# Kernel tuning notes

Measured on AMD Instinct MI355X. Metric: run time of the kernel, lower is better.

## Reference

```python
import jax, jax.numpy as jnp
import numpy as np

B, L, D = 2, 4096, 1024
H, DK, DV = 4, 256, 256
CONV_K = 4
FIR_KS = (1, 3, 7, 15)
GQP = 128
NS = len(FIR_KS) + 2  # fir scales + delta path + direct value path
GIN = GQP + NS
GH = max(8, GIN)
CHUNK = 32
FLOOR = 0.02  # step 0 -> floor_start


def l2norm(x):
    return x * jax.lax.rsqrt(jnp.sum(x * x, -1, keepdims=True) + 1e-6)


def dw_causal_conv(x, w):
    # x: (B, L, C), w: (C, K) depthwise causal conv (ShortConvolution / FIR)
    K = w.shape[1]
    y = jax.lax.conv_general_dilated(
        jnp.moveaxis(x, 1, 2), w[:, None, :], (1,), [(K - 1, 0)],
        feature_group_count=w.shape[0],
        dimension_numbers=("NCH", "OIH", "NCH"))
    return jnp.moveaxis(y, 1, 2)


def delta_rule_chunkwise(q, k, v, beta):
    # q,k: (b,h,L,dk)  v: (b,h,L,dv)  beta: (b,h,L);  L % CHUNK == 0
    b, h, Lp, dk = q.shape
    dv = v.shape[-1]
    n = Lp // CHUNK
    q = l2norm(q)
    k = l2norm(k)
    v = v * beta[..., None]
    kb = k * beta[..., None]
    rs = lambda t: t.reshape(b, h, n, CHUNK, -1)
    q, k, v, kb = rs(q), rs(k), rs(v), rs(kb)
    tri = jnp.triu(jnp.ones((CHUNK, CHUNK), bool), 0)       # incl diag
    tri_s = jnp.triu(jnp.ones((CHUNK, CHUNK), bool), 1)     # strict upper
    # inv = -(k_beta k^T) masked to strictly-lower
    inv = -jnp.where(tri, 0.0, jnp.einsum('bhncd,bhned->bhnce', kb, k))
    # forward substitution: (I - A)^{-1} - I for strictly lower A
    for i in range(1, CHUNK):
        row = inv[:, :, :, i, :]                              # (b,h,n,C)
        upd = jnp.einsum('bhnk,bhnkj->bhnj', row, inv)        # zero for j>=i
        inv = inv.at[:, :, :, i, :].add(upd)
    inv = inv + jnp.eye(CHUNK, dtype=inv.dtype)
    inv = inv.astype(jnp.bfloat16).astype(q.dtype)
    u = inv @ v                                               # (b,h,n,C,dv)
    w = inv @ kb                                              # (b,h,n,C,dk)
    mv = lambda t: jnp.moveaxis(t, 2, 0)                      # -> (n,b,h,C,d)
    S0 = jnp.zeros((b, h, dk, dv), q.dtype)

    def step(S, xs):
        q_i, k_i, u_i, w_i = xs
        attn = jnp.where(tri_s, 0.0, q_i @ jnp.swapaxes(k_i, -1, -2))
        u_t = u_i - w_i @ S
        o = q_i @ S + attn @ u_t
        S = S + jnp.swapaxes(k_i, -1, -2) @ u_t
        return S, o

    _, out = jax.lax.scan(step, S0, (mv(q), mv(k), mv(u), mv(w)))
    return jnp.moveaxis(out, 0, 2).reshape(b, h, Lp, dv)


def rmsnorm(x, w, eps=1e-5):
    return x * jax.lax.rsqrt(jnp.mean(x * x, -1, keepdims=True) + eps) * w


def _dirac_fir(key, channels, k):
    w = jnp.zeros((channels, k), jnp.float32).at[:, -1].set(1.0)
    return w + 0.01 * jax.random.normal(key, (channels, k), jnp.float32)


def setup_inputs():
    key = jax.random.key(0)
    ks = jax.random.split(key, 24)
    sc = 0.02
    C = H * DV
    b2 = jnp.zeros((NS,), jnp.float32).at[-1].set(1.0)  # identity-path bias
    return {
        "hidden_states": jax.random.normal(ks[0], (B, L, D), jnp.float32),
        "Wq": jax.random.normal(ks[1], (D, H * DK), jnp.float32) * sc,
        "Wk": jax.random.normal(ks[2], (D, H * DK), jnp.float32) * sc,
        "Wv": jax.random.normal(ks[3], (D, H * DV), jnp.float32) * sc,
        "Wb": jax.random.normal(ks[4], (D, H), jnp.float32) * sc,
        "conv_q_w": jax.random.normal(ks[5], (H * DK, CONV_K), jnp.float32) * 0.1,
        "conv_k_w": jax.random.normal(ks[6], (H * DK, CONV_K), jnp.float32) * 0.1,
        "conv_v_w": jax.random.normal(ks[7], (H * DV, CONV_K), jnp.float32) * 0.1,
        "fir_w0": _dirac_fir(ks[8], C, FIR_KS[0]),
        "fir_w1": _dirac_fir(ks[9], C, FIR_KS[1]),
        "fir_w2": _dirac_fir(ks[10], C, FIR_KS[2]),
        "fir_w3": _dirac_fir(ks[11], C, FIR_KS[3]),
        "Wqg": jax.random.normal(ks[12], (D, GQP), jnp.float32) * sc,
        "bqg": jnp.zeros((GQP,), jnp.float32),
        "Wf1": jax.random.normal(ks[13], (GIN, GH), jnp.float32) * sc,
        "bf1": jnp.zeros((GH,), jnp.float32),
        "Wf2": jax.random.normal(ks[14], (GH, NS), jnp.float32) * sc,
        "bf2": b2,
        "log_temp": jnp.zeros((H,), jnp.float32),
        "o_norm_w": jnp.ones((DV,), jnp.float32),
        "Wo": jax.random.normal(ks[15], (H * DV, D), jnp.float32) * sc,
    }


def reference(hidden_states, Wq, Wk, Wv, Wb, conv_q_w, conv_k_w, conv_v_w,
              fir_w0, fir_w1, fir_w2, fir_w3, Wqg, bqg, Wf1, bf1, Wf2, bf2,
              log_temp, o_norm_w, Wo):
    x = hidden_states
    # projections + causal ShortConvolution with SiLU (qk_activation='silu')
    q = jax.nn.silu(dw_causal_conv(x @ Wq, conv_q_w))
    k = jax.nn.silu(dw_causal_conv(x @ Wk, conv_k_w))
    v = jax.nn.silu(dw_causal_conv(x @ Wv, conv_v_w))
    q = q.reshape(B, L, H, DK)
    k = k.reshape(B, L, H, DK)
    v_direct = v.reshape(B, L, H, DV)
    beta = jax.nn.sigmoid(x @ Wb)  # (B,L,H)
    bh = lambda t: jnp.swapaxes(t, 1, 2)  # (B,L,H,d) -> (B,H,L,d)
    delta_bh = delta_rule_chunkwise(bh(q), bh(k), bh(v_direct), jnp.swapaxes(beta, 1, 2))
    delta_out = jnp.swapaxes(delta_bh, 1, 2)  # (B,L,H,DV)
    # multi-scale depthwise causal FIR branches on the value stream
    v_flat = v_direct.reshape(B, L, H * DV)
    firs = [dw_causal_conv(v_flat, w).reshape(B, L, H, DV)
            for w in (fir_w0, fir_w1, fir_w2, fir_w3)]
    streams = jnp.stack(firs + [delta_out, v_direct], axis=3)  # (B,L,H,NS,DV)
    # query-conditioned summary router
    summaries = jnp.mean(streams, axis=-1)                     # (B,L,H,NS)
    qg = x @ Wqg + bqg                                         # (B,L,GQP)
    qg = jnp.broadcast_to(qg[:, :, None, :], (B, L, H, GQP))
    gate_in = jnp.concatenate([qg, summaries], axis=-1)        # (B,L,H,GIN)
    hmid = jax.nn.gelu(gate_in @ Wf1 + bf1, approximate=False)
    logits = (hmid @ Wf2 + bf2) / jnp.exp(log_temp)[None, None, :, None]
    p = jax.nn.softmax(logits, axis=-1)
    p = p * (1.0 - NS * FLOOR) + FLOOR                          # prob floor
    fused = jnp.einsum('blhs,blhsd->blhd', p, streams)
    o = rmsnorm(fused, o_norm_w)
    return o.reshape(B, L, H * DV) @ Wo
```

## Files before the change

### kernel.cpp

```cpp
#include <hip/hip_runtime.h>
#include <hip/hip_bf16.h>
#include <math.h>

#define B_ 2
#define L_ 4096
#define D_ 1024
#define H_ 4
#define DK_ 256
#define BL_ 8192
#define C_ 1024
#define NCH_ 128
#define GQP_c 128
#define NS_c 6
#define GIN_c 134
#define GH_c 134

typedef __attribute__((ext_vector_type(8))) short short8;
typedef __attribute__((ext_vector_type(4))) float f32x4;

__device__ __forceinline__ float block_sum256(float v, float* red) {
  int t = threadIdx.x;
  #pragma unroll
  for (int o = 32; o > 0; o >>= 1) v += __shfl_down(v, o, 64);
  __syncthreads();
  if ((t & 63) == 0) red[t >> 6] = v;
  __syncthreads();
  return red[0] + red[1] + red[2] + red[3];
}

__device__ __forceinline__ unsigned short bf16bits(float f) {
  __hip_bfloat16 h = __float2bfloat16(f);
  return *(unsigned short*)&h;
}

__device__ __forceinline__ float bits2f(unsigned short u) {
  unsigned int x = ((unsigned int)u) << 16;
  return *(float*)&x;
}

__device__ __forceinline__ float4 fma4(float4 a, float4 b, float4 c) {
  return make_float4(fmaf(a.x, b.x, c.x), fmaf(a.y, b.y, c.y),
                     fmaf(a.z, b.z, c.z), fmaf(a.w, b.w, c.w));
}

__device__ __forceinline__ void gload_lds16(const void* g, void* l) {
  __builtin_amdgcn_global_load_lds(
      (const __attribute__((address_space(1))) void*)g,
      (__attribute__((address_space(3))) void*)l, 16, 0, 0);
}

__global__ __launch_bounds__(256) void f32_to_bf16_k(const float* __restrict__ in,
    __hip_bfloat16* __restrict__ out) {
  size_t i = ((size_t)blockIdx.x * 256 + threadIdx.x) << 2;
  float4 v = *(const float4*)(in + i);
  ushort4 o;
  o.x = bf16bits(v.x); o.y = bf16bits(v.y); o.z = bf16bits(v.z); o.w = bf16bits(v.w);
  *(ushort4*)((unsigned short*)out + i) = o;
}

__global__ __launch_bounds__(256) void transpose_bf16(const float* __restrict__ W,
    __hip_bfloat16* __restrict__ WT, int K, int N) {
  __shared__ float tile[32][33];
  int t = threadIdx.x;
  int r = t >> 3, c4 = (t & 7) << 2;
  int n0 = blockIdx.x << 5, k0 = blockIdx.y << 5;
  float4 v = *(const float4*)(W + (size_t)(k0 + r) * N + n0 + c4);
  tile[r][c4] = v.x; tile[r][c4 + 1] = v.y; tile[r][c4 + 2] = v.z; tile[r][c4 + 3] = v.w;
  __syncthreads();
  ushort4 o;
  o.x = bf16bits(tile[c4][r]);
  o.y = bf16bits(tile[c4 + 1][r]);
  o.z = bf16bits(tile[c4 + 2][r]);
  o.w = bf16bits(tile[c4 + 3][r]);
  *(ushort4*)((unsigned short*)WT + (size_t)(n0 + r) * K + k0 + c4) = o;
}

__global__ __launch_bounds__(256) void small_transpose(const float* __restrict__ in,
    float* __restrict__ out, int R, int Cc, int OS) {
  int total = Cc * OS;
  for (int e = blockIdx.x * 256 + threadIdx.x; e < total; e += gridDim.x * 256) {
    int cIdx = e / OS, r = e - cIdx * OS;
    out[e] = (r < R) ? in[(size_t)r * Cc + cIdx] : 0.f;
  }
}

__global__ __launch_bounds__(256) void wf1q_prep(const float* __restrict__ Wf1,
    __hip_bfloat16* __restrict__ out) {
  int idx = blockIdx.x * 256 + threadIdx.x;
  int u = idx >> 7, i = idx & 127;
  float val = (u < GH_c) ? Wf1[i * GH_c + u] : 0.f;
  out[idx] = __float2bfloat16(val);
}

__global__ __launch_bounds__(256) void conv_prep(const float* __restrict__ cw,
    float* __restrict__ cwT) {
  int t = blockIdx.x * 256 + threadIdx.x;
  int j = t >> 10, c = t & (C_ - 1);
  cwT[t] = cw[(c << 2) + j];
}

__global__ __launch_bounds__(256) void gemm_bf16(
    const __hip_bfloat16* __restrict__ A, const __hip_bfloat16* __restrict__ BT,
    const float* __restrict__ bias, float* __restrict__ C, int M, int N, int K) {
  __shared__ __align__(16) __hip_bfloat16 Asm[4096];
  __shared__ __align__(16) __hip_bfloat16 Bsm[4096];
  int tid = threadIdx.x;
  int lane = tid & 63, wave = tid >> 6;
  int wm = wave >> 1, wn = wave & 1;
  int rowBase = blockIdx.y * 128, colBase = blockIdx.x * 128;
  f32x4 acc[4][4];
  #pragma unroll
  for (int i = 0; i < 4; ++i)
    #pragma unroll
    for (int j = 0; j < 4; ++j) acc[i][j] = (f32x4){0.f, 0.f, 0.f, 0.f};

  for (int kt = 0; kt < K; kt += 32) {
    __syncthreads();
    #pragma unroll
    for (int it = 0; it < 2; ++it) {
      int s = tid + (it << 8);
      int T = s >> 6, q = (s >> 4) & 3, m = s & 15;
      const __hip_bfloat16* ga = A + (size_t)(rowBase + T * 16 + m) * K + kt + q * 8;
      gload_lds16(ga, Asm + s * 8);
      const __hip_bfloat16* gb = BT + (size_t)(colBase + T * 16 + m) * K + kt + q * 8;
      gload_lds16(gb, Bsm + s * 8);
    }
    __syncthreads();
    short8 af[4], bfr[4];
    #pragma unroll
    for (int i = 0; i < 4; ++i) {
      af[i]  = *(const short8*)(Asm + ((wm * 4 + i) << 9) + lane * 8);
      bfr[i] = *(const short8*)(Bsm + ((wn * 4 + i) << 9) + lane * 8);
    }
    #pragma unroll
    for (int i = 0; i < 4; ++i)
      #pragma unroll
      for (int j = 0; j < 4; ++j)
        acc[i][j] = __builtin_amdgcn_mfma_f32_16x16x32_bf16(af[i], bfr[j], acc[i][j], 0, 0, 0);
  }
  int r0 = (lane >> 4) * 4, c0 = lane & 15;
  #pragma unroll
  for (int i = 0; i < 4; ++i) {
    int row = rowBase + (wm * 4 + i) * 16 + r0;
    #pragma unroll
    for (int j = 0; j < 4; ++j) {
      int col = colBase + (wn * 4 + j) * 16 + c0;
      float bs = bias ? bias[col] : 0.f;
      #pragma unroll
      for (int r = 0; r < 4; ++r)
        C[(size_t)(row + r) * N + col] = acc[i][j][r] + bs;
    }
  }
}

__global__ __launch_bounds__(256) void conv_silu_v4(const float* __restrict__ in,
    const float* __restrict__ wT, float* __restrict__ out) {
  int f = blockIdx.x * 256 + threadIdx.x;
  int e = f << 2;
  int c = e & (C_ - 1);
  int l = (e >> 10) & (L_ - 1);
  float4 acc = make_float4(0.f, 0.f, 0.f, 0.f);
  #pragma unroll
  for (int j = 0; j < 4; ++j) {
    int ll = l - 3 + j;
    if (ll >= 0) {
      float4 vj = *(const float4*)(in + e + ((j - 3) << 10));
      float4 wj = *(const float4*)(wT + (j << 10) + c);
      acc = fma4(wj, vj, acc);
    }
  }
  float4 o;
  o.x = acc.x / (1.f + expf(-acc.x));
  o.y = acc.y / (1.f + expf(-acc.y));
  o.z = acc.z / (1.f + expf(-acc.z));
  o.w = acc.w / (1.f + expf(-acc.w));
  *(float4*)(out + e) = o;
}

__global__ __launch_bounds__(256) void beta_kernel(const float* __restrict__ x,
    const float* __restrict__ Wb, float* __restrict__ beta) {
  int row = blockIdx.x;
  int t = threadIdx.x;
  int h = t >> 6, lane = t & 63;
  const float* xr = x + (size_t)row * D_;
  float acc = 0.f;
  for (int k = lane; k < D_; k += 64) acc += xr[k] * Wb[(k << 2) + h];
  #pragma unroll
  for (int o = 32; o > 0; o >>= 1) acc += __shfl_down(acc, o, 64);
  if (lane == 0) beta[(row << 2) + h] = 1.f / (1.f + expf(-acc));
}

__global__ __launch_bounds__(256) void precompute(const float* __restrict__ q,
    const float* __restrict__ k, const float* __restrict__ v,
    const float* __restrict__ beta,
    float* __restrict__ qn, float* __restrict__ kn,
    float* __restrict__ vb, float* __restrict__ kb) {
  __shared__ float red[4];
  int bid = blockIdx.x;
  int t = threadIdx.x;
  int b = bid >> 14;
  int h = (bid >> 12) & 3;
  int l = bid & (L_ - 1);
  size_t in_off = (((size_t)(b * L_ + l)) << 10) + (h << 8) + t;
  float qv = q[in_off], kv = k[in_off], vv = v[in_off];
  float sq = block_sum256(qv * qv, red);
  float sk = block_sum256(kv * kv, red);
  float rq = rsqrtf(sq + 1e-6f);
  float rk = rsqrtf(sk + 1e-6f);
  float bt = beta[((b * L_ + l) << 2) + h];
  size_t oo = ((size_t)bid << 8) + t;
  float knv = kv * rk;
  qn[oo] = qv * rq;
  kn[oo] = knv;
  vb[oo] = vv * bt;
  kb[oo] = knv * bt;
}

__global__ __launch_bounds__(256) void inv_attn(const float* __restrict__ qn,
    const float* kn, const float* __restrict__ kb,
    float* __restrict__ invb, __hip_bfloat16* __restrict__ att_bf,
    __hip_bfloat16* knT_bf) {
  __shared__ float kn_s[32][257];
  __shared__ float inv_s[32][33];
  int ci = blockIdx.x;
  int t = threadIdx.x;
  size_t base = ((size_t)ci) << 13;
  for (int e = t; e < 8192; e += 256) kn_s[e >> 8][e & 255] = kn[base + e];
  __syncthreads();
  {
    unsigned short tmp[32];
    #pragma unroll
    for (int j = 0; j < 32; ++j) tmp[j] = bf16bits(kn_s[j][t]);
    unsigned short* kd = (unsigned short*)knT_bf + (((size_t)ci) << 14) +
                         (size_t)(t >> 4) * 512 + (size_t)(t & 15) * 8;
    #pragma unroll
    for (int g = 0; g < 4; ++g) *(uint4*)(kd + g * 128) = ((const uint4*)tmp)[g];
  }
  {
    int r = t >> 3, kt = t & 7;
    const float4* qrow = (const float4*)(qn + base + (size_t)r * 256 + (kt << 5));
    unsigned short tmp[32];
    #pragma unroll
    for (int i = 0; i < 8; ++i) {
      float4 f = qrow[i];
      tmp[i * 4 + 0] = bf16bits(f.x); tmp[i * 4 + 1] = bf16bits(f.y);
      tmp[i * 4 + 2] = bf16bits(f.z); tmp[i * 4 + 3] = bf16bits(f.w);
    }
    unsigned short* qd = (unsigned short*)knT_bf + (((size_t)ci) << 14) + 8192 +
                         (size_t)(((r >> 4) << 3) + kt) * 512 + (size_t)(r & 15) * 8;
    #pragma unroll
    for (int g = 0; g < 4; ++g) *(uint4*)(qd + g * 128) = ((const uint4*)tmp)[g];
  }
  #pragma unroll
  for (int p = 0; p < 4; ++p) {
    int e = t + (p << 8);
    int i = e >> 5, j = e & 31;
    const float* kbi = kb + base + (i << 8);
    const float* qni = qn + base + (i << 8);
    float am = 0.f, aa = 0.f;
    for (int kk = 0; kk < 256; ++kk) {
      float knv = kn_s[j][kk];
      am += kbi[kk] * knv;
      aa += qni[kk] * knv;
    }
    inv_s[i][j] = (j < i) ? -am : 0.f;
    ((unsigned short*)att_bf)[((size_t)ci << 10) + (size_t)(i >> 4) * 512 +
        (size_t)((i & 15) + ((j >> 3) << 4)) * 8 + (j & 7)] =
        bf16bits((j <= i) ? aa : 0.f);
  }
  __syncthreads();
  for (int i = 1; i < 32; ++i) {
    float upd = 0.f;
    if (t < i) {
      for (int kk = t + 1; kk < i; ++kk) upd += inv_s[i][kk] * inv_s[kk][t];
    }
    __syncthreads();
    if (t < i) inv_s[i][t] += upd;
    __syncthreads();
  }
  #pragma unroll
  for (int p = 0; p < 4; ++p) {
    int e = t + (p << 8);
    int i = e >> 5, j = e & 31;
    float val = inv_s[i][j] + (i == j ? 1.f : 0.f);
    val = __bfloat162float(__float2bfloat16(val));
    invb[((size_t)ci << 10) + e] = val;
  }
}

__global__ __launch_bounds__(256) void uw_kernel(const float* __restrict__ invb,
    float* __restrict__ vb_u, float* kb_w, __hip_bfloat16* w_bf) {
  __shared__ float inv_s[32][33];
  __shared__ float tile[32][260];
  int ci = blockIdx.x, t = threadIdx.x;
  size_t base = ((size_t)ci) << 13;
  for (int e = t; e < 1024; e += 256) inv_s[e >> 5][e & 31] = invb[((size_t)ci << 10) + e];
  for (int ph = 0; ph < 2; ++ph) {
    const float* src = (ph == 0) ? vb_u : kb_w;
    __syncthreads();
    for (int f = t; f < 2048; f += 256) {
      int e = f << 2;
      *(float4*)&tile[e >> 8][e & 255] = *(const float4*)(src + base + e);
    }
    __syncthreads();
    int c4 = (t & 63) << 2;
    int ig = t >> 6;
    float4 acc[8];
    #pragma unroll
    for (int ii = 0; ii < 8; ++ii) acc[ii] = make_float4(0.f, 0.f, 0.f, 0.f);
    for (int j = 0; j < 32; ++j) {
      float4 v4 = *(const float4*)&tile[j][c4];
      #pragma unroll
      for (int ii = 0; ii < 8; ++ii) {
        float iv = inv_s[(ig << 3) + ii][j];
        acc[ii].x += iv * v4.x; acc[ii].y += iv * v4.y;
        acc[ii].z += iv * v4.z; acc[ii].w += iv * v4.w;
      }
    }
    #pragma unroll
    for (int ii = 0; ii < 8; ++ii) {
      int i = (ig << 3) + ii;
      if (ph == 0) {
        *(float4*)(vb_u + base + (i << 8) + c4) = acc[ii];
      } else {
        ushort4 o;
        o.x = bf16bits(-acc[ii].x); o.y = bf16bits(-acc[ii].y);
        o.z = bf16bits(-acc[ii].z); o.w = bf16bits(-acc[ii].w);
        unsigned short* wd = (unsigned short*)w_bf + (((size_t)ci) << 14) +
            (size_t)(((i >> 4) << 3) + (c4 >> 5)) * 512 +
            (size_t)((i & 15) + (((c4 >> 3) & 3) << 4)) * 8 + (c4 & 7);
        *(ushort4*)wd = o;
      }
    }
  }
}

__global__ __launch_bounds__(64, 1) void scan_kernel(
    const __hip_bfloat16* __restrict__ w_bf,
    const __hip_bfloat16* __restrict__ kq_bf,
    const __hip_bfloat16* __restrict__ att_bf,
    const float* __restrict__ u, float* __restrict__ dout) {
  __shared__ __align__(16) unsigned short Sim[2][2][16 * 264];
  __shared__ __align__(16) float UtT[16 * 36];
  int lane = threadIdx.x;
  int mlane = lane & 15, quad = lane >> 4;
  int bh = blockIdx.x & 7;
  int cb = blockIdx.x >> 3;
  int cbase = cb << 4;

  const unsigned short* wbase = (const unsigned short*)w_bf;
  const unsigned short* kqbase = (const unsigned short*)kq_bf;
  const unsigned short* abase = (const unsigned short*)att_bf;

  short8 Wr[16], Qr[16], Kr[16], Ar[2];
  float ur[8], urn[8];

  auto load_WQ = [&](int nc) {
    size_t cb14 = ((size_t)(bh * NCH_ + nc)) << 14;
    const short8* wg = (const short8*)(wbase + cb14 + (size_t)lane * 8);
    const short8* qg = (const short8*)(kqbase + cb14 + 8192 + (size_t)lane * 8);
    #pragma unroll
    for (int s = 0; s < 16; ++s) { Wr[s] = wg[s * 64]; Qr[s] = qg[s * 64]; }
  };
  auto load_K = [&](int nc) {
    size_t cb14 = ((size_t)(bh * NCH_ + nc)) << 14;
    const short8* kg = (const short8*)(kqbase + cb14 + (size_t)lane * 8);
    #pragma unroll
    for (int s = 0; s < 16; ++s) Kr[s] = kg[s * 64];
  };
  auto load_A = [&](int nc) {
    const short8* ag = (const short8*)(abase + (((size_t)(bh * NCH_ + nc)) << 10) +
                                       (size_t)lane * 8);
    Ar[0] = ag[0]; Ar[1] = ag[64];
  };
  auto load_u8 = [&](int nc, float* dst) {
    size_t cbf = ((size_t)(bh * NCH_ + nc)) << 13;
    const float* up = u + cbf + (size_t)(quad * 4) * 256 + cbase + mlane;
    #pragma unroll
    for (int tt = 0; tt < 2; ++tt)
      #pragma unroll
      for (int r = 0; r < 4; ++r) dst[tt * 4 + r] = up[(tt * 16 + r) * 256];
  };

  for (int e = lane; e < 16 * 264; e += 64) { Sim[0][0][e] = 0; Sim[0][1][e] = 0; }
  f32x4 accS[16];
  #pragma unroll
  for (int i = 0; i < 16; ++i) accS[i] = (f32x4){0.f, 0.f, 0.f, 0.f};

  load_WQ(0);
  load_K(0);
  load_A(0);
  load_u8(0, ur);

  for (int nc = 0; nc < NCH_; ++nc) {
    int cur = nc & 1, alt = cur ^ 1;
    int nn = nc + 1 < NCH_ ? nc + 1 : NCH_ - 1;

    f32x4 uh0 = (f32x4){ur[0], ur[1], ur[2], ur[3]};
    f32x4 uh1 = (f32x4){ur[4], ur[5], ur[6], ur[7]};
    f32x4 ul0 = (f32x4){0.f, 0.f, 0.f, 0.f}, ul1 = (f32x4){0.f, 0.f, 0.f, 0.f};
    f32x4 oh0 = (f32x4){0.f, 0.f, 0.f, 0.f}, oh1 = (f32x4){0.f, 0.f, 0.f, 0.f};
    f32x4 ol0 = (f32x4){0.f, 0.f, 0.f, 0.f}, ol1 = (f32x4){0.f, 0.f, 0.f, 0.f};
    #pragma unroll
    for (int kt = 0; kt < 8; ++kt) {
      short8 bhi = *(const short8*)&Sim[cur][0][mlane * 264 + kt * 32 + quad * 8];
      short8 blo = *(const short8*)&Sim[cur][1][mlane * 264 + kt * 32 + quad * 8];
      uh0 = __builtin_amdgcn_mfma_f32_16x16x32_bf16(Wr[kt], bhi, uh0, 0, 0, 0);
      ul0 = __builtin_amdgcn_mfma_f32_16x16x32_bf16(Wr[kt], blo, ul0, 0, 0, 0);
      uh1 = __builtin_amdgcn_mfma_f32_16x16x32_bf16(Wr[8 + kt], bhi, uh1, 0, 0, 0);
      ul1 = __builtin_amdgcn_mfma_f32_16x16x32_bf16(Wr[8 + kt], blo, ul1, 0, 0, 0);
      oh0 = __builtin_amdgcn_mfma_f32_16x16x32_bf16(Qr[kt], bhi, oh0, 0, 0, 0);
      ol0 = __builtin_amdgcn_mfma_f32_16x16x32_bf16(Qr[kt], blo, ol0, 0, 0, 0);
      oh1 = __builtin_amdgcn_mfma_f32_16x16x32_bf16(Qr[8 + kt], bhi, oh1, 0, 0, 0);
      ol1 = __builtin_amdgcn_mfma_f32_16x16x32_bf16(Qr[8 + kt], blo, ol1, 0, 0, 0);
    }
    f32x4 ut0 = uh0 + ul0, ut1 = uh1 + ul1;
    *(f32x4*)&UtT[mlane * 36 + quad * 4] = ut0;
    *(f32x4*)&UtT[mlane * 36 + 16 + quad * 4] = ut1;
    load_WQ(nn);
    load_u8(nn, urn);
    short8 but;
    {
      const float* up = &UtT[mlane * 36 + quad * 8];
      #pragma unroll
      for (int j = 0; j < 8; ++j) but[j] = (short)bf16bits(up[j]);
    }
    f32x4 o0 = oh0 + ol0, o1 = oh1 + ol1;
    o0 = __builtin_amdgcn_mfma_f32_16x16x32_bf16(Ar[0], but, o0, 0, 0, 0);
    o1 = __builtin_amdgcn_mfma_f32_16x16x32_bf16(Ar[1], but, o1, 0, 0, 0);
    load_A(nn);
    size_t cbf = ((size_t)(bh * NCH_ + nc)) << 13;
    float* op = dout + cbf + (size_t)(quad * 4) * 256 + cbase + mlane;
    #pragma unroll
    for (int r = 0; r < 4; ++r) { op[r * 256] = o0[r]; op[(16 + r) * 256] = o1[r]; }
    #pragma unroll
    for (int t2 = 0; t2 < 16; ++t2) {
      accS[t2] = __builtin_amdgcn_mfma_f32_16x16x32_bf16(Kr[t2], but, accS[t2], 0, 0, 0);
      unsigned short nh[4], nl[4];
      #pragma unroll
      for (int r = 0; r < 4; ++r) {
        float sv = accS[t2][r];
        unsigned short hb = bf16bits(sv);
        nh[r] = hb;
        nl[r] = bf16bits(sv - bits2f(hb));
      }
      *(uint2*)&Sim[alt][0][mlane * 264 + t2 * 16 + quad * 4] = *(const uint2*)nh;
      *(uint2*)&Sim[alt][1][mlane * 264 + t2 * 16 + quad * 4] = *(const uint2*)nl;
    }
    load_K(nn);
    #pragma unroll
    for (int r = 0; r < 8; ++r) ur[r] = urn[r];
  }
}

__global__ __launch_bounds__(256, 1) void gate_kernel(
    const float* __restrict__ v, const float* __restrict__ delta,
    const float* __restrict__ qgH,
    const float* __restrict__ fw0, const float* __restrict__ fw1T,
    const float* __restrict__ fw2T, const float* __restrict__ fw3T,
    const float* __restrict__ Wf1, const float* __restrict__ Wf2,
    const float* __restrict__ bf1, const float* __restrict__ bf2,
    const float* __restrict__ ltm, const float* __restrict__ onw,
    __hip_bfloat16* __restrict__ obf) {
  __shared__ float W1t[6][136];
  __shared__ float W2f[804];
  __shared__ float bf1s[136];
  int t = threadIdx.x;
  int wave = t >> 6, lane = t & 63;
  for (int e = t; e < 804; e += 256) {
    int s = e / 134, u = e - s * 134;
    W1t[s][u] = Wf1[(128 + s) * GH_c + u];
    W2f[e] = Wf2[e];
  }
  if (t < GH_c) bf1s[t] = bf1[t];
  __syncthreads();

  int bid = blockIdx.x;
  int bl0 = (((bid & 7) << 7) | (bid >> 3)) << 3;
  int b = bl0 >> 12;
  int h = wave;
  int c = (h << 8) + (lane << 2);

  float4 fw3r[15], fw2r[7], fw1r[3], fw0r;
  #pragma unroll
  for (int j = 0; j < 15; ++j) fw3r[j] = *(const float4*)(fw3T + (j << 10) + c);
  #pragma unroll
  for (int j = 0; j < 7; ++j) fw2r[j] = *(const float4*)(fw2T + (j << 10) + c);
  #pragma unroll
  for (int j = 0; j < 3; ++j) fw1r[j] = *(const float4*)(fw1T + (j << 10) + c);
  fw0r = *(const float4*)(fw0 + c);
  float4 ow = *(const float4*)(onw + (lane << 2));
  float itemp = expf(ltm[h]);
  float b2r[6];
  #pragma unroll
  for (int s = 0; s < 6; ++s) b2r[s] = bf2[s];
  int u3 = 128 + (lane < 6 ? lane : 0);

  auto gelu = [](float a) -> float {
    return 0.5f * a * (1.f + erff(a * 0.70710678f));
  };

  for (int tk = 0; tk < 8; ++tk) {
    int bl = bl0 + tk;
    int l = bl & (L_ - 1);
    float4 st0, st1, st2, st3, st4, st5;
    st1 = make_float4(0, 0, 0, 0);
    st2 = make_float4(0, 0, 0, 0);
    st3 = make_float4(0, 0, 0, 0);
    #pragma unroll
    for (int j = 0; j < 15; ++j) {
      int ll = l - 14 + j;
      float4 vj = make_float4(0, 0, 0, 0);
      if (ll >= 0) vj = *(const float4*)(v + ((((size_t)(b * L_ + ll)) << 10) + c));
      st3 = fma4(fw3r[j], vj, st3);
      if (j >= 8) st2 = fma4(fw2r[j - 8], vj, st2);
      if (j >= 12) st1 = fma4(fw1r[j - 12], vj, st1);
      if (j == 14) {
        st0 = make_float4(fw0r.x * vj.x, fw0r.y * vj.y, fw0r.z * vj.z, fw0r.w * vj.w);
        st5 = vj;
      }
    }
    st4 = *(const float4*)(delta + ((((size_t)((b * H_ + h) * L_ + l)) << 8) + (lane << 2)));

    float s0 = st0.x + st0.y + st0.z + st0.w;
    float s1 = st1.x + st1.y + st1.z + st1.w;
    float s2 = st2.x + st2.y + st2.z + st2.w;
    float s3 = st3.x + st3.y + st3.z + st3.w;
    float s4 = st4.x + st4.y + st4.z + st4.w;
    float s5 = st5.x + st5.y + st5.z + st5.w;
    #pragma unroll
    for (int o = 32; o > 0; o >>= 1) {
      s0 += __shfl_down(s0, o, 64); s1 += __shfl_down(s1, o, 64);
      s2 += __shfl_down(s2, o, 64); s3 += __shfl_down(s3, o, 64);
      s4 += __shfl_down(s4, o, 64); s5 += __shfl_down(s5, o, 64);
    }
    float ss_[6];
    ss_[0] = __shfl(s0, 0, 64) * (1.f / 256.f);
    ss_[1] = __shfl(s1, 0, 64) * (1.f / 256.f);
    ss_[2] = __shfl(s2, 0, 64) * (1.f / 256.f);
    ss_[3] = __shfl(s3, 0, 64) * (1.f / 256.f);
    ss_[4] = __shfl(s4, 0, 64) * (1.f / 256.f);
    ss_[5] = __shfl(s5, 0, 64) * (1.f / 256.f);

    const float* qr = qgH + ((size_t)bl << 8);
    float a0 = qr[lane] + bf1s[lane];
    float a1 = qr[64 + lane] + bf1s[64 + lane];
    float a2 = qr[u3] + bf1s[u3];
    #pragma unroll
    for (int s = 0; s < 6; ++s) {
      a0 = fmaf(W1t[s][lane], ss_[s], a0);
      a1 = fmaf(W1t[s][64 + lane], ss_[s], a1);
      a2 = fmaf(W1t[s][u3], ss_[s], a2);
    }
    float h0 = gelu(a0);
    float h1 = gelu(a1);
    float h2 = (lane < 6) ? gelu(a2) : 0.f;

    const float* w2a = W2f + lane * 6;
    const float* w2b = W2f + (64 + lane) * 6;
    const float* w2c = W2f + u3 * 6;
    float t0 = h0 * w2a[0] + h1 * w2b[0] + h2 * w2c[0];
    float t1 = h0 * w2a[1] + h1 * w2b[1] + h2 * w2c[1];
    float t2 = h0 * w2a[2] + h1 * w2b[2] + h2 * w2c[2];
    float t3 = h0 * w2a[3] + h1 * w2b[3] + h2 * w2c[3];
    float t4 = h0 * w2a[4] + h1 * w2b[4] + h2 * w2c[4];
    float t5 = h0 * w2a[5] + h1 * w2b[5] + h2 * w2c[5];
    #pragma unroll
    for (int o = 32; o > 0; o >>= 1) {
      t0 += __shfl_down(t0, o, 64); t1 += __shfl_down(t1, o, 64);
      t2 += __shfl_down(t2, o, 64); t3 += __shfl_down(t3, o, 64);
      t4 += __shfl_down(t4, o, 64); t5 += __shfl_down(t5, o, 64);
    }
    float p0, p1, p2, p3, p4, p5;
    if (lane == 0) {
      float l0v = (t0 + b2r[0]) / itemp, l1v = (t1 + b2r[1]) / itemp;
      float l2v = (t2 + b2r[2]) / itemp, l3v = (t3 + b2r[3]) / itemp;
      float l4v = (t4 + b2r[4]) / itemp, l5v = (t5 + b2r[5]) / itemp;
      float m = fmaxf(fmaxf(fmaxf(l0v, l1v), fmaxf(l2v, l3v)), fmaxf(l4v, l5v));
      float e0 = expf(l0v - m), e1 = expf(l1v - m), e2 = expf(l2v - m);
      float e3 = expf(l3v - m), e4 = expf(l4v - m), e5 = expf(l5v - m);
      float inv = 1.f / (e0 + e1 + e2 + e3 + e4 + e5);
      p0 = e0 * inv * 0.88f + 0.02f; p1 = e1 * inv * 0.88f + 0.02f;
      p2 = e2 * inv * 0.88f + 0.02f; p3 = e3 * inv * 0.88f + 0.02f;
      p4 = e4 * inv * 0.88f + 0.02f; p5 = e5 * inv * 0.88f + 0.02f;
    }
    p0 = __shfl(p0, 0, 64); p1 = __shfl(p1, 0, 64); p2 = __shfl(p2, 0, 64);
    p3 = __shfl(p3, 0, 64); p4 = __shfl(p4, 0, 64); p5 = __shfl(p5, 0, 64);

    float4 fu;
    fu.x = p0 * st0.x + p1 * st1.x + p2 * st2.x + p3 * st3.x + p4 * st4.x + p5 * st5.x;
    fu.y = p0 * st0.y + p1 * st1.y + p2 * st2.y + p3 * st3.y + p4 * st4.y + p5 * st5.y;
    fu.z = p0 * st0.z + p1 * st1.z + p2 * st2.z + p3 * st3.z + p4 * st4.z + p5 * st5.z;
    fu.w = p0 * st0.w + p1 * st1.w + p2 * st2.w + p3 * st3.w + p4 * st4.w + p5 * st5.w;
    float ssq = fu.x * fu.x + fu.y * fu.y + fu.z * fu.z + fu.w * fu.w;
    #pragma unroll
    for (int o = 32; o > 0; o >>= 1) ssq += __shfl_xor(ssq, o, 64);
    float sc = rsqrtf(ssq * (1.f / 256.f) + 1e-5f);
    ushort4 ob;
    ob.x = bf16bits(fu.x * sc * ow.x);
    ob.y = bf16bits(fu.y * sc * ow.y);
    ob.z = bf16bits(fu.z * sc * ow.z);
    ob.w = bf16bits(fu.w * sc * ow.w);
    *(ushort4*)((unsigned short*)obf + (((size_t)bl) << 10) + c) = ob;
  }
}

extern "C" void kernel_launch(void* const* d_in, const int* in_sizes, int n_in,
                              void* d_out, int out_size, void* d_ws, size_t ws_size,
                              hipStream_t stream) {
  const float* x   = (const float*)d_in[0];
  const float* Wq  = (const float*)d_in[1];
  const float* Wk  = (const float*)d_in[2];
  const float* Wv  = (const float*)d_in[3];
  const float* Wb  = (const float*)d_in[4];
  const float* cqw = (const float*)d_in[5];
  const float* ckw = (const float*)d_in[6];
  const float* cvw = (const float*)d_in[7];
  const float* fw0 = (const float*)d_in[8];
  const float* fw1 = (const float*)d_in[9];
  const float* fw2 = (const float*)d_in[10];
  const float* fw3 = (const float*)d_in[11];
  const float* Wqg = (const float*)d_in[12];
  const float* bqg = (const float*)d_in[13];
  const float* Wf1 = (const float*)d_in[14];
  const float* bf1 = (const float*)d_in[15];
  const float* Wf2 = (const float*)d_in[16];
  const float* bf2 = (const float*)d_in[17];
  const float* ltm = (const float*)d_in[18];
  const float* onw = (const float*)d_in[19];
  const float* Wo  = (const float*)d_in[20];
  float* out = (float*)d_out;
  float* ws = (float*)d_ws;

  const size_t BIG = (size_t)BL_ * C_;
  float* qpre = ws;
  float* kpre = ws + BIG;
  float* vpre = ws + 2 * BIG;
  float* qs   = ws + 3 * BIG;
  float* ks   = ws + 4 * BIG;
  float* vs   = ws + 5 * BIG;
  float* kbw  = ws + 6 * BIG;
  float* invb = ws + 7 * BIG;
  float* attb = invb + (size_t)1024 * 1024;
  float* beta = attb + (size_t)1024 * 1024;
  float* qg   = beta + (size_t)BL_ * H_;

  __hip_bfloat16* x_bf  = (__hip_bfloat16*)qs;
  __hip_bfloat16* wqT   = (__hip_bfloat16*)kbw;
  __hip_bfloat16* wkT   = wqT + (size_t)1024 * 1024;
  __hip_bfloat16* wvT   = wkT + (size_t)1024 * 1024;
  __hip_bfloat16* wqgT  = wvT + (size_t)1024 * 1024;
  __hip_bfloat16* woT   = (__hip_bfloat16*)kbw;
  __hip_bfloat16* gate_bf = (__hip_bfloat16*)qpre;
  __hip_bfloat16* knT_bf = (__hip_bfloat16*)kpre;
  __hip_bfloat16* w_bf   = (__hip_bfloat16*)kbw;
  __hip_bfloat16* att_bf = (__hip_bfloat16*)attb;
  float* scr   = attb + (size_t)600000;
  float* fw1T  = scr;
  float* fw2T  = scr + 3072;
  float* fw3T  = scr + 10240;
  float* cqwT  = scr + 25600;
  float* ckwT  = scr + 29696;
  float* cvwT  = scr + 33792;

  float* qgH = ks;
  __hip_bfloat16* qg_bf  = (__hip_bfloat16*)(ks + (size_t)3 * 1024 * 1024);
  __hip_bfloat16* wf1qT  = (__hip_bfloat16*)(ks + (size_t)4 * 1024 * 1024);

  dim3 blk(256);
  f32_to_bf16_k<<<dim3(BL_ * D_ / 1024), blk, 0, stream>>>(x, x_bf);
  transpose_bf16<<<dim3(32, 32), blk, 0, stream>>>(Wq, wqT, D_, C_);
  transpose_bf16<<<dim3(32, 32), blk, 0, stream>>>(Wk, wkT, D_, C_);
  transpose_bf16<<<dim3(32, 32), blk, 0, stream>>>(Wv, wvT, D_, C_);
  transpose_bf16<<<dim3(4, 32), blk, 0, stream>>>(Wqg, wqgT, D_, GQP_c);
  small_transpose<<<dim3(16), blk, 0, stream>>>(fw1, fw1T, 1024, 3, 1024);
  small_transpose<<<dim3(32), blk, 0, stream>>>(fw2, fw2T, 1024, 7, 1024);
  small_transpose<<<dim3(64), blk, 0, stream>>>(fw3, fw3T, 1024, 15, 1024);
  conv_prep<<<dim3(16), blk, 0, stream>>>(cqw, cqwT);
  conv_prep<<<dim3(16), blk, 0, stream>>>(ckw, ckwT);
  conv_prep<<<dim3(16), blk, 0, stream>>>(cvw, cvwT);
  gemm_bf16<<<dim3(8, 64), blk, 0, stream>>>(x_bf, wqT, nullptr, qpre, BL_, C_, D_);
  gemm_bf16<<<dim3(8, 64), blk, 0, stream>>>(x_bf, wkT, nullptr, kpre, BL_, C_, D_);
  gemm_bf16<<<dim3(8, 64), blk, 0, stream>>>(x_bf, wvT, nullptr, vpre, BL_, C_, D_);
  gemm_bf16<<<dim3(1, 64), blk, 0, stream>>>(x_bf, wqgT, bqg, qg, BL_, GQP_c, D_);
  beta_kernel<<<dim3(BL_), blk, 0, stream>>>(x, Wb, beta);
  conv_silu_v4<<<dim3(BL_ * C_ / 1024), blk, 0, stream>>>(qpre, cqwT, qs);
  conv_silu_v4<<<dim3(BL_ * C_ / 1024), blk, 0, stream>>>(kpre, ckwT, ks);
  conv_silu_v4<<<dim3(BL_ * C_ / 1024), blk, 0, stream>>>(vpre, cvwT, vs);
  precompute<<<dim3(B_ * H_ * L_), blk, 0, stream>>>(qs, ks, vs, beta, qpre, kpre,
                                                     vpre, kbw);
  f32_to_bf16_k<<<dim3(BL_ * GQP_c / 1024), blk, 0, stream>>>(qg, qg_bf);
  wf1q_prep<<<dim3(128), blk, 0, stream>>>(Wf1, wf1qT);
  gemm_bf16<<<dim3(2, 64), blk, 0, stream>>>(qg_bf, wf1qT, nullptr, qgH, BL_, 256, 128);
  inv_attn<<<dim3(1024), blk, 0, stream>>>(qpre, kpre, kbw, invb, att_bf, knT_bf);
  uw_kernel<<<dim3(1024), blk, 0, stream>>>(invb, vpre, kbw, w_bf);
  scan_kernel<<<dim3(128), dim3(64), 0, stream>>>(w_bf, knT_bf, att_bf, vpre, qs);
  transpose_bf16<<<dim3(32, 32), blk, 0, stream>>>(Wo, woT, C_, D_);
  gate_kernel<<<dim3(1024), blk, 0, stream>>>(vs, qs, qgH, fw0, fw1T, fw2T, fw3T,
                                              Wf1, Wf2, bf1, bf2, ltm, onw, gate_bf);
  gemm_bf16<<<dim3(8, 64), blk, 0, stream>>>(gate_bf, woT, nullptr, out, BL_, D_, C_);
}
```

Measured before the change: 943.8 us.

## Fuse causal conv, SiLU and L2 norm; apply beta on the fly downstream

```diff
diff --git a/kernel.cpp b/kernel.cpp
--- a/kernel.cpp
+++ b/kernel.cpp
@@ -18,16 +18,6 @@
 typedef __attribute__((ext_vector_type(8))) short short8;
 typedef __attribute__((ext_vector_type(4))) float f32x4;
 
-__device__ __forceinline__ float block_sum256(float v, float* red) {
-  int t = threadIdx.x;
-  #pragma unroll
-  for (int o = 32; o > 0; o >>= 1) v += __shfl_down(v, o, 64);
-  __syncthreads();
-  if ((t & 63) == 0) red[t >> 6] = v;
-  __syncthreads();
-  return red[0] + red[1] + red[2] + red[3];
-}
-
 __device__ __forceinline__ unsigned short bf16bits(float f) {
   __hip_bfloat16 h = __float2bfloat16(f);
   return *(unsigned short*)&h;
@@ -41,6 +31,11 @@
 __device__ __forceinline__ float4 fma4(float4 a, float4 b, float4 c) {
   return make_float4(fmaf(a.x, b.x, c.x), fmaf(a.y, b.y, c.y),
                      fmaf(a.z, b.z, c.z), fmaf(a.w, b.w, c.w));
+}
+
+__device__ __forceinline__ float4 silu4(float4 a) {
+  return make_float4(a.x / (1.f + expf(-a.x)), a.y / (1.f + expf(-a.y)),
+                     a.z / (1.f + expf(-a.z)), a.w / (1.f + expf(-a.w)));
 }
 
 __device__ __forceinline__ void gload_lds16(const void* g, void* l) {
@@ -153,30 +148,6 @@
   }
 }
 
-__global__ __launch_bounds__(256) void conv_silu_v4(const float* __restrict__ in,
-    const float* __restrict__ wT, float* __restrict__ out) {
-  int f = blockIdx.x * 256 + threadIdx.x;
-  int e = f << 2;
-  int c = e & (C_ - 1);
-  int l = (e >> 10) & (L_ - 1);
-  float4 acc = make_float4(0.f, 0.f, 0.f, 0.f);
-  #pragma unroll
-  for (int j = 0; j < 4; ++j) {
-    int ll = l - 3 + j;
-    if (ll >= 0) {
-      float4 vj = *(const float4*)(in + e + ((j - 3) << 10));
-      float4 wj = *(const float4*)(wT + (j << 10) + c);
-      acc = fma4(wj, vj, acc);
-    }
-  }
-  float4 o;
-  o.x = acc.x / (1.f + expf(-acc.x));
-  o.y = acc.y / (1.f + expf(-acc.y));
-  o.z = acc.z / (1.f + expf(-acc.z));
-  o.w = acc.w / (1.f + expf(-acc.w));
-  *(float4*)(out + e) = o;
-}
-
 __global__ __launch_bounds__(256) void beta_kernel(const float* __restrict__ x,
     const float* __restrict__ Wb, float* __restrict__ beta) {
   int row = blockIdx.x;
@@ -190,41 +161,59 @@
   if (lane == 0) beta[(row << 2) + h] = 1.f / (1.f + expf(-acc));
 }
 
-__global__ __launch_bounds__(256) void precompute(const float* __restrict__ q,
-    const float* __restrict__ k, const float* __restrict__ v,
-    const float* __restrict__ beta,
-    float* __restrict__ qn, float* __restrict__ kn,
-    float* __restrict__ vb, float* __restrict__ kb) {
-  __shared__ float red[4];
+__global__ __launch_bounds__(256) void conv_norm_fused(
+    const float* __restrict__ qpre, const float* __restrict__ kpre,
+    const float* __restrict__ vpre,
+    const float* __restrict__ cqwT, const float* __restrict__ ckwT,
+    const float* __restrict__ cvwT,
+    float* __restrict__ vs, float* __restrict__ qn, float* __restrict__ kn) {
   int bid = blockIdx.x;
+  int b = bid >> 12, l = bid & (L_ - 1);
   int t = threadIdx.x;
-  int b = bid >> 14;
-  int h = (bid >> 12) & 3;
-  int l = bid & (L_ - 1);
-  size_t in_off = (((size_t)(b * L_ + l)) << 10) + (h << 8) + t;
-  float qv = q[in_off], kv = k[in_off], vv = v[in_off];
-  float sq = block_sum256(qv * qv, red);
-  float sk = block_sum256(kv * kv, red);
-  float rq = rsqrtf(sq + 1e-6f);
-  float rk = rsqrtf(sk + 1e-6f);
-  float bt = beta[((b * L_ + l) << 2) + h];
-  size_t oo = ((size_t)bid << 8) + t;
-  float knv = kv * rk;
-  qn[oo] = qv * rq;
-  kn[oo] = knv;
-  vb[oo] = vv * bt;
-  kb[oo] = knv * bt;
+  int h = t >> 6, lane = t & 63;
+  int c = t << 2;
+  float4 qa = make_float4(0.f, 0.f, 0.f, 0.f);
+  float4 ka = make_float4(0.f, 0.f, 0.f, 0.f);
+  float4 va = make_float4(0.f, 0.f, 0.f, 0.f);
+  #pragma unroll
+  for (int j = 0; j < 4; ++j) {
+    int ll = l - 3 + j;
+    if (ll >= 0) {
+      size_t roff = (((size_t)(b * L_ + ll)) << 10) + c;
+      qa = fma4(*(const float4*)(cqwT + (j << 10) + c), *(const float4*)(qpre + roff), qa);
+      ka = fma4(*(const float4*)(ckwT + (j << 10) + c), *(const float4*)(kpre + roff), ka);
+      va = fma4(*(const float4*)(cvwT + (j << 10) + c), *(const float4*)(vpre + roff), va);
+    }
+  }
+  float4 qv = silu4(qa), kv = silu4(ka), vv = silu4(va);
+  *(float4*)(vs + (((size_t)bid) << 10) + c) = vv;
+  float sq = qv.x * qv.x + qv.y * qv.y + qv.z * qv.z + qv.w * qv.w;
+  float sk = kv.x * kv.x + kv.y * kv.y + kv.z * kv.z + kv.w * kv.w;
+  #pragma unroll
+  for (int o = 32; o > 0; o >>= 1) {
+    sq += __shfl_xor(sq, o, 64);
+    sk += __shfl_xor(sk, o, 64);
+  }
+  float rq = rsqrtf(sq + 1e-6f), rk = rsqrtf(sk + 1e-6f);
+  size_t oo = ((((size_t)(b * H_ + h)) * L_ + l) << 8) + (lane << 2);
+  float4 qo = make_float4(qv.x * rq, qv.y * rq, qv.z * rq, qv.w * rq);
+  float4 ko = make_float4(kv.x * rk, kv.y * rk, kv.z * rk, kv.w * rk);
+  *(float4*)(qn + oo) = qo;
+  *(float4*)(kn + oo) = ko;
 }
 
 __global__ __launch_bounds__(256) void inv_attn(const float* __restrict__ qn,
-    const float* kn, const float* __restrict__ kb,
+    const float* kn, const float* __restrict__ beta,
     float* __restrict__ invb, __hip_bfloat16* __restrict__ att_bf,
     __hip_bfloat16* knT_bf) {
   __shared__ float kn_s[32][257];
   __shared__ float inv_s[32][33];
+  __shared__ float bt_s[32];
   int ci = blockIdx.x;
   int t = threadIdx.x;
   size_t base = ((size_t)ci) << 13;
+  int bb = ci >> 9, hh = (ci >> 7) & 3, nc = ci & 127;
+  if (t < 32) bt_s[t] = beta[(((size_t)(bb * L_ + nc * 32 + t)) << 2) + hh];
   for (int e = t; e < 8192; e += 256) kn_s[e >> 8][e & 255] = kn[base + e];
   __syncthreads();
   {
@@ -255,12 +244,13 @@
   for (int p = 0; p < 4; ++p) {
     int e = t + (p << 8);
     int i = e >> 5, j = e & 31;
-    const float* kbi = kb + base + (i << 8);
+    const float* kni = kn + base + (i << 8);
     const float* qni = qn + base + (i << 8);
+    float bti = bt_s[i];
     float am = 0.f, aa = 0.f;
     for (int kk = 0; kk < 256; ++kk) {
       float knv = kn_s[j][kk];
-      am += kbi[kk] * knv;
+      am += (kni[kk] * bti) * knv;
       aa += qni[kk] * knv;
     }
     inv_s[i][j] = (j < i) ? -am : 0.f;
@@ -289,18 +279,29 @@
 }
 
 __global__ __launch_bounds__(256) void uw_kernel(const float* __restrict__ invb,
-    float* __restrict__ vb_u, float* kb_w, __hip_bfloat16* w_bf) {
+    const float* __restrict__ vs, const float* __restrict__ kn,
+    const float* __restrict__ beta,
+    float* __restrict__ u_out, __hip_bfloat16* w_bf) {
   __shared__ float inv_s[32][33];
   __shared__ float tile[32][260];
+  __shared__ float bt_s[32];
   int ci = blockIdx.x, t = threadIdx.x;
   size_t base = ((size_t)ci) << 13;
+  int bb = ci >> 9, hh = (ci >> 7) & 3, nc = ci & 127;
+  size_t vbase = (((size_t)(bb * L_ + nc * 32)) << 10) + (hh << 8);
   for (int e = t; e < 1024; e += 256) inv_s[e >> 5][e & 31] = invb[((size_t)ci << 10) + e];
+  if (t < 32) bt_s[t] = beta[(((size_t)(bb * L_ + nc * 32 + t)) << 2) + hh];
   for (int ph = 0; ph < 2; ++ph) {
-    const float* src = (ph == 0) ? vb_u : kb_w;
     __syncthreads();
     for (int f = t; f < 2048; f += 256) {
       int e = f << 2;
-      *(float4*)&tile[e >> 8][e & 255] = *(const float4*)(src + base + e);
+      int i = e >> 8, d = e & 255;
+      float4 v4;
+      if (ph == 0) v4 = *(const float4*)(vs + vbase + (size_t)i * 1024 + d);
+      else         v4 = *(const float4*)(kn + base + (i << 8) + d);
+      float bt = bt_s[i];
+      v4.x *= bt; v4.y *= bt; v4.z *= bt; v4.w *= bt;
+      *(float4*)&tile[i][d] = v4;
     }
     __syncthreads();
     int c4 = (t & 63) << 2;
@@ -321,7 +322,7 @@
     for (int ii = 0; ii < 8; ++ii) {
       int i = (ig << 3) + ii;
       if (ph == 0) {
-        *(float4*)(vb_u + base + (i << 8) + c4) = acc[ii];
+        *(float4*)(u_out + base + (i << 8) + c4) = acc[ii];
       } else {
         ushort4 o;
         o.x = bf16bits(-acc[ii].x); o.y = bf16bits(-acc[ii].y);
@@ -684,16 +685,13 @@
   gemm_bf16<<<dim3(8, 64), blk, 0, stream>>>(x_bf, wvT, nullptr, vpre, BL_, C_, D_);
   gemm_bf16<<<dim3(1, 64), blk, 0, stream>>>(x_bf, wqgT, bqg, qg, BL_, GQP_c, D_);
   beta_kernel<<<dim3(BL_), blk, 0, stream>>>(x, Wb, beta);
-  conv_silu_v4<<<dim3(BL_ * C_ / 1024), blk, 0, stream>>>(qpre, cqwT, qs);
-  conv_silu_v4<<<dim3(BL_ * C_ / 1024), blk, 0, stream>>>(kpre, ckwT, ks);
-  conv_silu_v4<<<dim3(BL_ * C_ / 1024), blk, 0, stream>>>(vpre, cvwT, vs);
-  precompute<<<dim3(B_ * H_ * L_), blk, 0, stream>>>(qs, ks, vs, beta, qpre, kpre,
-                                                     vpre, kbw);
+  conv_norm_fused<<<dim3(BL_), blk, 0, stream>>>(qpre, kpre, vpre, cqwT, ckwT, cvwT,
+                                                 vs, qs, ks);
+  inv_attn<<<dim3(1024), blk, 0, stream>>>(qs, ks, beta, invb, att_bf, knT_bf);
+  uw_kernel<<<dim3(1024), blk, 0, stream>>>(invb, vs, ks, beta, vpre, w_bf);
   f32_to_bf16_k<<<dim3(BL_ * GQP_c / 1024), blk, 0, stream>>>(qg, qg_bf);
   wf1q_prep<<<dim3(128), blk, 0, stream>>>(Wf1, wf1qT);
   gemm_bf16<<<dim3(2, 64), blk, 0, stream>>>(qg_bf, wf1qT, nullptr, qgH, BL_, 256, 128);
-  inv_attn<<<dim3(1024), blk, 0, stream>>>(qpre, kpre, kbw, invb, att_bf, knT_bf);
-  uw_kernel<<<dim3(1024), blk, 0, stream>>>(invb, vpre, kbw, w_bf);
   scan_kernel<<<dim3(128), dim3(64), 0, stream>>>(w_bf, knT_bf, att_bf, vpre, qs);
   transpose_bf16<<<dim3(32, 32), blk, 0, stream>>>(Wo, woT, C_, D_);
   gate_kernel<<<dim3(1024), blk, 0, stream>>>(vs, qs, qgH, fw0, fw1T, fw2T, fw3T,
```

New measurement: 888.0 us. -5.9%, faster.
